# Optimization experiments

Measured on AMD Instinct MI355X. Metric: run time of the kernel, lower is better.

Reference implementation:

```python
import jax, jax.numpy as jnp
import numpy as np

B, L, H, E, K = 64, 200, 256, 8, 2
LN_EPS = 1e-5

def setup_inputs() -> dict:
    key = jax.random.key(0)
    ks = jax.random.split(key, 24)
    r = lambda k, *s: jax.random.normal(k, s, dtype=jnp.float32)
    w = lambda k, *s: 0.02 * jax.random.normal(k, s, dtype=jnp.float32)
    return {
        'text_emb': r(ks[0], B, L, H),
        'img_emb': r(ks[1], B, L, H),
        'item_emb': r(ks[2], B, L, H),
        'noise_t': r(ks[3], B, L, H),
        'noise_i': r(ks[4], B, L, H),
        'W_mu_t': w(ks[5], H, H), 'b_mu_t': jnp.zeros((H,), jnp.float32),
        'W_sg_t': w(ks[6], H, H), 'b_sg_t': jnp.zeros((H,), jnp.float32),
        'W_mu_i': w(ks[7], H, H), 'b_mu_i': jnp.zeros((H,), jnp.float32),
        'W_sg_i': w(ks[8], H, H), 'b_sg_i': jnp.zeros((H,), jnp.float32),
        'W_gate': w(ks[9], H, E), 'b_gate': jnp.zeros((E,), jnp.float32),
        'W_texp': w(ks[10], E, H, H), 'b_texp': jnp.zeros((E, H), jnp.float32),
        'W_iexp': w(ks[11], E, H, H), 'b_iexp': jnp.zeros((E, H), jnp.float32),
        'W_fuse': w(ks[12], 2 * H, H), 'b_fuse': jnp.zeros((H,), jnp.float32),
        'ln_g': jnp.ones((H,), jnp.float32), 'ln_b': jnp.zeros((H,), jnp.float32),
    }

def _topk_routing(z, W_gate, b_gate):
    # softmax over experts, keep top-k, renormalize (matches torch scatter_ version)
    weights = jax.nn.softmax(z @ W_gate + b_gate, axis=-1)   # [B,L,E]
    top_w, idx = jax.lax.top_k(weights, K)                   # [B,L,K]
    sparse = jnp.sum(jax.nn.one_hot(idx, E, dtype=weights.dtype) * top_w[..., None], axis=-2)
    return sparse / (jnp.sum(sparse, axis=-1, keepdims=True) + 1e-8)

def _layernorm(x, g, b):
    mu = jnp.mean(x, axis=-1, keepdims=True)
    var = jnp.mean(jnp.square(x - mu), axis=-1, keepdims=True)
    return (x - mu) * jax.lax.rsqrt(var + LN_EPS) * g + b

def reference(text_emb, img_emb, item_emb, noise_t, noise_i,
              W_mu_t, b_mu_t, W_sg_t, b_sg_t, W_mu_i, b_mu_i, W_sg_i, b_sg_i,
              W_gate, b_gate, W_texp, b_texp, W_iexp, b_iexp,
              W_fuse, b_fuse, ln_g, ln_b):
    # VAE-style reparameterization per modality
    t_mu = text_emb @ W_mu_t + b_mu_t
    t_sigma = jnp.exp(text_emb @ W_sg_t + b_sg_t)
    i_mu = img_emb @ W_mu_i + b_mu_i
    i_sigma = jnp.exp(img_emb @ W_sg_i + b_sg_i)
    t_z = t_mu + t_sigma * noise_t
    i_z = i_mu + i_sigma * noise_i
    # top-k gating
    t_gate = _topk_routing(t_z, W_gate, b_gate)   # [B,L,E]
    i_gate = _topk_routing(i_z, W_gate, b_gate)
    # dense all-expert stack + gated combine
    t_experts = jnp.einsum('blh,ehd->bled', t_z, W_texp) + b_texp  # [B,L,E,H]
    t_out = jnp.einsum('bled,ble->bld', t_experts, t_gate)
    i_experts = jnp.einsum('blh,ehd->bled', i_z, W_iexp) + b_iexp
    i_out = jnp.einsum('bled,ble->bld', i_experts, i_gate)
    # fusion: Linear(2H->H) -> LayerNorm -> ReLU, residual with item_emb
    cat = jnp.concatenate([t_out, i_out], axis=-1)
    fused = jax.nn.relu(_layernorm(cat @ W_fuse + b_fuse, ln_g, ln_b))
    fusion = item_emb + fused
    return fusion, t_mu, t_sigma, i_mu, i_sigma
```

## Files before the change

### kernel.cpp

```cpp
#include <hip/hip_runtime.h>
#include <hip/hip_bf16.h>
#include <math.h>

#define NTOK 12800
#define HD 256
#define SOUT (NTOK * HD)

typedef __attribute__((ext_vector_type(8))) short short8_t;
typedef __attribute__((ext_vector_type(4))) float f32x4;

__device__ __forceinline__ unsigned short f2b(float f) {
    union { float f; unsigned u; } v; v.f = f;
    unsigned r = (v.u + 0x7FFFu + ((v.u >> 16) & 1u)) >> 16;
    return (unsigned short)r;
}
__device__ __forceinline__ float b2f(unsigned short s) {
    union { unsigned u; float f; } v; v.u = ((unsigned)s) << 16;
    return v.f;
}

__global__ __launch_bounds__(256) void prepW_kernel(
    const float* __restrict__ W_texp, const float* __restrict__ W_iexp,
    const float* __restrict__ W_mu_t, const float* __restrict__ W_sg_t,
    const float* __restrict__ W_mu_i, const float* __restrict__ W_sg_i,
    const float* __restrict__ W_fuse,
    unsigned short* __restrict__ wt_t, unsigned short* __restrict__ wt_i,
    unsigned short* __restrict__ wt_f,
    unsigned short* __restrict__ wt_muth, unsigned short* __restrict__ wt_mutl,
    unsigned short* __restrict__ wt_sgth, unsigned short* __restrict__ wt_sgtl,
    unsigned short* __restrict__ wt_muih, unsigned short* __restrict__ wt_muil,
    unsigned short* __restrict__ wt_sgih, unsigned short* __restrict__ wt_sgil)
{
    const int z = blockIdx.y;
    const float* src;
    unsigned short* dsth;
    unsigned short* dstl = nullptr;
    int dstride = 256, koff = 0;
    if (z < 8)       { src = W_texp + (size_t)z * 65536;       dsth = wt_t + (size_t)z * 65536; }
    else if (z < 16) { src = W_iexp + (size_t)(z - 8) * 65536; dsth = wt_i + (size_t)(z - 8) * 65536; }
    else if (z == 16){ src = W_mu_t; dsth = wt_muth; dstl = wt_mutl; }
    else if (z == 17){ src = W_sg_t; dsth = wt_sgth; dstl = wt_sgtl; }
    else if (z == 18){ src = W_mu_i; dsth = wt_muih; dstl = wt_muil; }
    else if (z == 19){ src = W_sg_i; dsth = wt_sgih; dstl = wt_sgil; }
    else if (z == 20){ src = W_fuse;         dsth = wt_f; dstride = 512; koff = 0;   }
    else             { src = W_fuse + 65536; dsth = wt_f; dstride = 512; koff = 256; }

    const int tk = (blockIdx.x >> 2) * 64;
    const int td = (blockIdx.x & 3) * 64;
    __shared__ float T[64][68];
    const int t = threadIdx.x;
    {
        const int r = t >> 2, c0 = (t & 3) * 16;
        const float* s = &src[(size_t)(tk + r) * 256 + td + c0];
#pragma unroll
        for (int j = 0; j < 4; ++j)
            *reinterpret_cast<float4*>(&T[r][c0 + j * 4]) =
                *reinterpret_cast<const float4*>(&s[j * 4]);
    }
    __syncthreads();
    {
        const int d = t & 63, kc = (t >> 6) * 16;
        union { unsigned short s[16]; short8_t v[2]; } uh, ul;
#pragma unroll
        for (int j = 0; j < 16; ++j) {
            const float x = T[kc + j][d];
            uh.s[j] = f2b(x);
            ul.s[j] = f2b(x - b2f(uh.s[j]));
        }
        unsigned short* p = &dsth[(size_t)(td + d) * dstride + koff + tk + kc];
        *reinterpret_cast<short8_t*>(p) = uh.v[0];
        *reinterpret_cast<short8_t*>(p + 8) = uh.v[1];
        if (dstl) {
            unsigned short* q = &dstl[(size_t)(td + d) * 256 + tk + kc];
            *reinterpret_cast<short8_t*>(q) = ul.v[0];
            *reinterpret_cast<short8_t*>(q + 8) = ul.v[1];
        }
    }
}

__global__ __launch_bounds__(256) void reparam_mfma_kernel(
    const float* __restrict__ text, const float* __restrict__ img,
    const unsigned short* __restrict__ wt_muth, const unsigned short* __restrict__ wt_mutl,
    const unsigned short* __restrict__ wt_sgth, const unsigned short* __restrict__ wt_sgtl,
    const unsigned short* __restrict__ wt_muih, const unsigned short* __restrict__ wt_muil,
    const unsigned short* __restrict__ wt_sgih, const unsigned short* __restrict__ wt_sgil,
    const float* __restrict__ b_mu_t, const float* __restrict__ b_sg_t,
    const float* __restrict__ b_mu_i, const float* __restrict__ b_sg_i,
    const float* __restrict__ noise_t, const float* __restrict__ noise_i,
    float* __restrict__ o_tmu, float* __restrict__ o_tsig,
    float* __restrict__ o_imu, float* __restrict__ o_isig,
    unsigned short* __restrict__ tzb, unsigned short* __restrict__ izb)
{
    const int mod = blockIdx.z;
    const float* A            = mod ? img     : text;
    const unsigned short* Wmh = mod ? wt_muih : wt_muth;
    const unsigned short* Wml = mod ? wt_muil : wt_mutl;
    const unsigned short* Wsh = mod ? wt_sgih : wt_sgth;
    const unsigned short* Wsl = mod ? wt_sgil : wt_sgtl;
    const float* bmu          = mod ? b_mu_i  : b_mu_t;
    const float* bsg          = mod ? b_sg_i  : b_sg_t;
    const float* noise        = mod ? noise_i : noise_t;
    float* omu                = mod ? o_imu   : o_tmu;
    float* osg                = mod ? o_isig  : o_tsig;
    unsigned short* zb        = mod ? izb     : tzb;

    __shared__ __align__(16) unsigned short Ahs[4][128][8];
    __shared__ __align__(16) unsigned short Als[4][128][8];
    __shared__ __align__(16) unsigned short BMh[4][128][8];
    __shared__ __align__(16) unsigned short BMl[4][128][8];
    __shared__ __align__(16) unsigned short BSh[4][128][8];
    __shared__ __align__(16) unsigned short BSl[4][128][8];

    const int tid = threadIdx.x;
    const int lane = tid & 63;
    const int w = tid >> 6;
    const int wr = w >> 1, wc = w & 1;
    const int lg = lane >> 4;
    const int lr = lane & 15;
    const int m0 = blockIdx.x * 128;
    const int n0 = blockIdx.y * 128;

    f32x4 accM[4][4], accS[4][4];
#pragma unroll
    for (int mi = 0; mi < 4; ++mi)
#pragma unroll
        for (int ni = 0; ni < 4; ++ni) {
            accM[mi][ni] = (f32x4){0.f, 0.f, 0.f, 0.f};
            accS[mi][ni] = (f32x4){0.f, 0.f, 0.f, 0.f};
        }

    for (int ks = 0; ks < 8; ++ks) {
        __syncthreads();
        {
            const int r = tid >> 1, h = tid & 1;
            const float* s = &A[(size_t)(m0 + r) * HD + ks * 32 + h * 16];
#pragma unroll
            for (int j = 0; j < 2; ++j) {
                const float4 v0 = *reinterpret_cast<const float4*>(&s[j * 8]);
                const float4 v1 = *reinterpret_cast<const float4*>(&s[j * 8 + 4]);
                float x[8] = { v0.x, v0.y, v0.z, v0.w, v1.x, v1.y, v1.z, v1.w };
                union { unsigned short u[8]; short8_t v; } qh, ql;
#pragma unroll
                for (int c = 0; c < 8; ++c) {
                    qh.u[c] = f2b(x[c]);
                    ql.u[c] = f2b(x[c] - b2f(qh.u[c]));
                }
                *reinterpret_cast<short8_t*>(&Ahs[h * 2 + j][r][0]) = qh.v;
                *reinterpret_cast<short8_t*>(&Als[h * 2 + j][r][0]) = ql.v;
            }
        }
        {
            const int n = tid >> 1, h = tid & 1;
            const size_t wo = (size_t)(n0 + n) * HD + ks * 32 + h * 16;
#pragma unroll
            for (int j = 0; j < 2; ++j) {
                *reinterpret_cast<short8_t*>(&BMh[2 * h + j][n][0]) =
                    *reinterpret_cast<const short8_t*>(&Wmh[wo + j * 8]);
                *reinterpret_cast<short8_t*>(&BMl[2 * h + j][n][0]) =
                    *reinterpret_cast<const short8_t*>(&Wml[wo + j * 8]);
                *reinterpret_cast<short8_t*>(&BSh[2 * h + j][n][0]) =
                    *reinterpret_cast<const short8_t*>(&Wsh[wo + j * 8]);
                *reinterpret_cast<short8_t*>(&BSl[2 * h + j][n][0]) =
                    *reinterpret_cast<const short8_t*>(&Wsl[wo + j * 8]);
            }
        }
        __syncthreads();

        short8_t ahf[4], alf[4];
#pragma unroll
        for (int mi = 0; mi < 4; ++mi) {
            ahf[mi] = *reinterpret_cast<const short8_t*>(&Ahs[lg][wr * 64 + mi * 16 + lr][0]);
            alf[mi] = *reinterpret_cast<const short8_t*>(&Als[lg][wr * 64 + mi * 16 + lr][0]);
        }
#pragma unroll
        for (int ni = 0; ni < 4; ++ni) {
            const short8_t bmh = *reinterpret_cast<const short8_t*>(&BMh[lg][wc * 64 + ni * 16 + lr][0]);
            const short8_t bml = *reinterpret_cast<const short8_t*>(&BMl[lg][wc * 64 + ni * 16 + lr][0]);
            const short8_t bsh = *reinterpret_cast<const short8_t*>(&BSh[lg][wc * 64 + ni * 16 + lr][0]);
            const short8_t bsl = *reinterpret_cast<const short8_t*>(&BSl[lg][wc * 64 + ni * 16 + lr][0]);
#pragma unroll
            for (int mi = 0; mi < 4; ++mi) {
                accM[mi][ni] = __builtin_amdgcn_mfma_f32_16x16x32_bf16(ahf[mi], bmh, accM[mi][ni], 0, 0, 0);
                accM[mi][ni] = __builtin_amdgcn_mfma_f32_16x16x32_bf16(ahf[mi], bml, accM[mi][ni], 0, 0, 0);
                accM[mi][ni] = __builtin_amdgcn_mfma_f32_16x16x32_bf16(alf[mi], bmh, accM[mi][ni], 0, 0, 0);
                accS[mi][ni] = __builtin_amdgcn_mfma_f32_16x16x32_bf16(ahf[mi], bsh, accS[mi][ni], 0, 0, 0);
                accS[mi][ni] = __builtin_amdgcn_mfma_f32_16x16x32_bf16(ahf[mi], bsl, accS[mi][ni], 0, 0, 0);
                accS[mi][ni] = __builtin_amdgcn_mfma_f32_16x16x32_bf16(alf[mi], bsh, accS[mi][ni], 0, 0, 0);
            }
        }
    }

    float bm[4], bs[4];
    int cc[4];
#pragma unroll
    for (int ni = 0; ni < 4; ++ni) {
        cc[ni] = n0 + wc * 64 + ni * 16 + lr;
        bm[ni] = bmu[cc[ni]];
        bs[ni] = bsg[cc[ni]];
    }
#pragma unroll
    for (int mi = 0; mi < 4; ++mi) {
#pragma unroll
        for (int r = 0; r < 4; ++r) {
            const int row = m0 + wr * 64 + mi * 16 + lg * 4 + r;
#pragma unroll
            for (int ni = 0; ni < 4; ++ni) {
                const size_t off = (size_t)row * HD + cc[ni];
                const float mu = accM[mi][ni][r] + bm[ni];
                const float sg = expf(accS[mi][ni][r] + bs[ni]);
                omu[off] = mu;
                osg[off] = sg;
                zb[off] = f2b(fmaf(sg, noise[off], mu));
            }
        }
    }
}

__global__ __launch_bounds__(256) void gate_kernel(
    const float* __restrict__ mu, const float* __restrict__ sig,
    const float* __restrict__ noise, const float* __restrict__ Wg,
    const float* __restrict__ bg, float* __restrict__ gate)
{
    const int lane = threadIdx.x & 63;
    const int n = blockIdx.x * 4 + (threadIdx.x >> 6);
    const size_t off = (size_t)n * HD + lane * 4;
    const float4 m4 = *reinterpret_cast<const float4*>(&mu[off]);
    const float4 s4 = *reinterpret_cast<const float4*>(&sig[off]);
    const float4 n4 = *reinterpret_cast<const float4*>(&noise[off]);
    const float zz[4] = { fmaf(s4.x, n4.x, m4.x), fmaf(s4.y, n4.y, m4.y),
                          fmaf(s4.z, n4.z, m4.z), fmaf(s4.w, n4.w, m4.w) };
    float lg[8];
#pragma unroll
    for (int e = 0; e < 8; ++e) lg[e] = 0.f;
#pragma unroll
    for (int i = 0; i < 4; ++i) {
        const float* wr = &Wg[(size_t)(lane * 4 + i) * 8];
        const float4 w0 = *reinterpret_cast<const float4*>(wr);
        const float4 w1 = *reinterpret_cast<const float4*>(wr + 4);
        lg[0] = fmaf(zz[i], w0.x, lg[0]); lg[1] = fmaf(zz[i], w0.y, lg[1]);
        lg[2] = fmaf(zz[i], w0.z, lg[2]); lg[3] = fmaf(zz[i], w0.w, lg[3]);
        lg[4] = fmaf(zz[i], w1.x, lg[4]); lg[5] = fmaf(zz[i], w1.y, lg[5]);
        lg[6] = fmaf(zz[i], w1.z, lg[6]); lg[7] = fmaf(zz[i], w1.w, lg[7]);
    }
#pragma unroll
    for (int off2 = 32; off2; off2 >>= 1)
#pragma unroll
        for (int e = 0; e < 8; ++e) lg[e] += __shfl_down(lg[e], off2);

    if (lane == 0) {
        float m = -1e30f;
#pragma unroll
        for (int e = 0; e < 8; ++e) { lg[e] += bg[e]; m = fmaxf(m, lg[e]); }
        float p[8], s = 0.f;
// ... 13 lines not shown
#pragma unroll
        for (int e = 0; e < 8; ++e) g[e] = 0.f;
        g[e1] = p[e1] * denom; g[e2] = p[e2] * denom;
        float* gr = &gate[(size_t)n * 8];
        *reinterpret_cast<float4*>(gr)     = make_float4(g[0], g[1], g[2], g[3]);
        *reinterpret_cast<float4*>(gr + 4) = make_float4(g[4], g[5], g[6], g[7]);
    }
}

__global__ __launch_bounds__(256) void expert_mfma_kernel(
    const unsigned short* __restrict__ tzb, const unsigned short* __restrict__ izb,
    const unsigned short* __restrict__ wt_t, const unsigned short* __restrict__ wt_i,
    const float* __restrict__ bx_t, const float* __restrict__ bx_i,
    const float* __restrict__ g_t, const float* __restrict__ g_i,
    unsigned short* __restrict__ out_t, unsigned short* __restrict__ out_i)
{
    const int mod = blockIdx.z;
    const unsigned short* Zb = mod ? izb : tzb;
    const unsigned short* Wt = mod ? wt_i : wt_t;
    const float* bx   = mod ? bx_i : bx_t;
    const float* gate = mod ? g_i  : g_t;
    unsigned short* outp = mod ? out_i : out_t;

    __shared__ __align__(16) unsigned short Al[32][128][8];
    __shared__ __align__(16) unsigned short Bl[4][128][8];
    __shared__ float gld[128][8];

    const int tid = threadIdx.x;
    const int lane = tid & 63;
    const int w = tid >> 6;
    const int wr = w >> 1, wc = w & 1;
    const int lg = lane >> 4;
    const int lr = lane & 15;
    const int m0 = blockIdx.x * 128;
    const int n0 = blockIdx.y * 128;

    reinterpret_cast<float4*>(&gld[0][0])[tid] =
        reinterpret_cast<const float4*>(&gate[(size_t)m0 * 8])[tid];

    {
        const int r = tid >> 1, h = tid & 1;
        const unsigned short* src = &Zb[(size_t)(m0 + r) * HD + h * 128];
#pragma unroll
        for (int j = 0; j < 16; ++j)
            *reinterpret_cast<short8_t*>(&Al[h * 16 + j][r][0]) =
                *reinterpret_cast<const short8_t*>(&src[j * 8]);
    }
    __syncthreads();

    f32x4 accT[4][4];
#pragma unroll
    for (int mi = 0; mi < 4; ++mi)
#pragma unroll
        for (int ni = 0; ni < 4; ++ni)
            accT[mi][ni] = (f32x4){0.f, 0.f, 0.f, 0.f};

    for (int e = 0; e < 8; ++e) {
        f32x4 acc[4][4];
#pragma unroll
        for (int mi = 0; mi < 4; ++mi)
#pragma unroll
            for (int ni = 0; ni < 4; ++ni)
                acc[mi][ni] = (f32x4){0.f, 0.f, 0.f, 0.f};

        const unsigned short* We = &Wt[(size_t)e * HD * HD + (size_t)n0 * HD];

        for (int ks = 0; ks < 8; ++ks) {
            __syncthreads();
            {
                const int n = tid >> 1, h = tid & 1;
                const unsigned short* s = &We[(size_t)n * HD + ks * 32 + h * 16];
                *reinterpret_cast<short8_t*>(&Bl[2 * h][n][0]) =
                    *reinterpret_cast<const short8_t*>(&s[0]);
                *reinterpret_cast<short8_t*>(&Bl[2 * h + 1][n][0]) =
                    *reinterpret_cast<const short8_t*>(&s[8]);
            }
            __syncthreads();

            short8_t af[4], bf[4];
#pragma unroll
            for (int mi = 0; mi < 4; ++mi)
                af[mi] = *reinterpret_cast<const short8_t*>(
                    &Al[ks * 4 + lg][wr * 64 + mi * 16 + lr][0]);
#pragma unroll
            for (int ni = 0; ni < 4; ++ni)
                bf[ni] = *reinterpret_cast<const short8_t*>(
                    &Bl[lg][wc * 64 + ni * 16 + lr][0]);
#pragma unroll
            for (int mi = 0; mi < 4; ++mi)
#pragma unroll
                for (int ni = 0; ni < 4; ++ni)
                    acc[mi][ni] = __builtin_amdgcn_mfma_f32_16x16x32_bf16(
                        af[mi], bf[ni], acc[mi][ni], 0, 0, 0);
        }

#pragma unroll
        for (int mi = 0; mi < 4; ++mi) {
            const int rb = wr * 64 + mi * 16 + lg * 4;
            const float gv0 = gld[rb + 0][e];
            const float gv1 = gld[rb + 1][e];
            const float gv2 = gld[rb + 2][e];
            const float gv3 = gld[rb + 3][e];
#pragma unroll
            for (int ni = 0; ni < 4; ++ni) {
                const float bv = bx[(size_t)e * HD + n0 + wc * 64 + ni * 16 + lr];
                accT[mi][ni][0] += gv0 * (acc[mi][ni][0] + bv);
                accT[mi][ni][1] += gv1 * (acc[mi][ni][1] + bv);
                accT[mi][ni][2] += gv2 * (acc[mi][ni][2] + bv);
                accT[mi][ni][3] += gv3 * (acc[mi][ni][3] + bv);
            }
        }
    }

#pragma unroll
    for (int mi = 0; mi < 4; ++mi)
#pragma unroll
        for (int ni = 0; ni < 4; ++ni)
#pragma unroll
            for (int r = 0; r < 4; ++r)
                outp[(size_t)(m0 + wr * 64 + mi * 16 + lg * 4 + r) * HD
                     + n0 + wc * 64 + ni * 16 + lr] = f2b(accT[mi][ni][r]);
}

__global__ __launch_bounds__(256) void fusegemm_mfma_kernel(
    const unsigned short* __restrict__ t_outb, const unsigned short* __restrict__ i_outb,
    const unsigned short* __restrict__ wtf, const float* __restrict__ bfuse,
    float* __restrict__ fused)
{
    __shared__ __align__(16) unsigned short Al[8][128][8];
    __shared__ __align__(16) unsigned short Bl[8][128][8];

    const int tid = threadIdx.x;
    const int lane = tid & 63;
    const int w = tid >> 6;
    const int wr = w >> 1, wc = w & 1;
    const int lg = lane >> 4;
    const int lr = lane & 15;
    const int m0 = blockIdx.x * 128;
    const int n0 = blockIdx.y * 128;

    f32x4 acc[4][4];
#pragma unroll
    for (int mi = 0; mi < 4; ++mi)
#pragma unroll
        for (int ni = 0; ni < 4; ++ni)
            acc[mi][ni] = (f32x4){0.f, 0.f, 0.f, 0.f};

    for (int ks = 0; ks < 8; ++ks) {
        __syncthreads();
        {
            const int r = tid >> 1, h = tid & 1;
            const unsigned short* base = (ks < 4) ? t_outb : i_outb;
            const int kloc = (ks & 3) * 64 + h * 32;
            const unsigned short* s = &base[(size_t)(m0 + r) * HD + kloc];
#pragma unroll
            for (int j = 0; j < 4; ++j)
                *reinterpret_cast<short8_t*>(&Al[h * 4 + j][r][0]) =
                    *reinterpret_cast<const short8_t*>(&s[j * 8]);
        }
        {
            const int n = tid >> 1, h = tid & 1;
            const unsigned short* s = &wtf[(size_t)(n0 + n) * 512 + ks * 64 + h * 32];
#pragma unroll
            for (int j = 0; j < 4; ++j)
                *reinterpret_cast<short8_t*>(&Bl[h * 4 + j][n][0]) =
                    *reinterpret_cast<const short8_t*>(&s[j * 8]);
        }
        __syncthreads();

#pragma unroll
        for (int kc = 0; kc < 2; ++kc) {
            short8_t af[4], bf[4];
#pragma unroll
            for (int mi = 0; mi < 4; ++mi)
                af[mi] = *reinterpret_cast<const short8_t*>(
                    &Al[kc * 4 + lg][wr * 64 + mi * 16 + lr][0]);
#pragma unroll
            for (int ni = 0; ni < 4; ++ni)
                bf[ni] = *reinterpret_cast<const short8_t*>(
                    &Bl[kc * 4 + lg][wc * 64 + ni * 16 + lr][0]);
#pragma unroll
            for (int mi = 0; mi < 4; ++mi)
#pragma unroll
                for (int ni = 0; ni < 4; ++ni)
                    acc[mi][ni] = __builtin_amdgcn_mfma_f32_16x16x32_bf16(
                        af[mi], bf[ni], acc[mi][ni], 0, 0, 0);
        }
    }

    float bv[4];
    int cc[4];
#pragma unroll
    for (int ni = 0; ni < 4; ++ni) {
        cc[ni] = n0 + wc * 64 + ni * 16 + lr;
        bv[ni] = bfuse[cc[ni]];
    }
#pragma unroll
    for (int mi = 0; mi < 4; ++mi)
#pragma unroll
        for (int r = 0; r < 4; ++r) {
            const int row = m0 + wr * 64 + mi * 16 + lg * 4 + r;
#pragma unroll
            for (int ni = 0; ni < 4; ++ni)
                fused[(size_t)row * HD + cc[ni]] = acc[mi][ni][r] + bv[ni];
        }
}

__global__ __launch_bounds__(256) void ln_relu_res_kernel(
    const float* __restrict__ fused, const float* __restrict__ g,
    const float* __restrict__ b, const float* __restrict__ item,
    float* __restrict__ fusion)
{
    const int lane = threadIdx.x & 63;
    const int n = blockIdx.x * 4 + (threadIdx.x >> 6);
    const size_t off = (size_t)n * HD + lane * 4;
    const float4 x = *reinterpret_cast<const float4*>(&fused[off]);
    float s = x.x + x.y + x.z + x.w;
    float ss = x.x * x.x + x.y * x.y + x.z * x.z + x.w * x.w;
#pragma unroll
    for (int o = 32; o; o >>= 1) { s += __shfl_xor(s, o); ss += __shfl_xor(ss, o); }
    const float mean = s * (1.f / 256.f);
    const float var = ss * (1.f / 256.f) - mean * mean;
    const float rstd = rsqrtf(var + 1e-5f);
    const float4 gg = *reinterpret_cast<const float4*>(&g[lane * 4]);
// ... 22 lines not shown
    const float* b_sg_t  = (const float*)d_in[8];
    const float* W_mu_i  = (const float*)d_in[9];
    const float* b_mu_i  = (const float*)d_in[10];
    const float* W_sg_i  = (const float*)d_in[11];
    const float* b_sg_i  = (const float*)d_in[12];
    const float* W_gate  = (const float*)d_in[13];
    const float* b_gate  = (const float*)d_in[14];
    const float* W_texp  = (const float*)d_in[15];
    const float* b_texp  = (const float*)d_in[16];
    const float* W_iexp  = (const float*)d_in[17];
    const float* b_iexp  = (const float*)d_in[18];
    const float* W_fuse  = (const float*)d_in[19];
    const float* b_fuse  = (const float*)d_in[20];
    const float* ln_g    = (const float*)d_in[21];
    const float* ln_b    = (const float*)d_in[22];

    float* out    = (float*)d_out;
    float* fusion = out;
    float* o_tmu  = out + (size_t)SOUT;
    float* o_tsig = out + (size_t)2 * SOUT;
    float* o_imu  = out + (size_t)3 * SOUT;
    float* o_isig = out + (size_t)4 * SOUT;

    float* ws     = (float*)d_ws;
    float* fused  = ws;
    float* t_gate = ws + (size_t)SOUT;
    float* i_gate = t_gate + (size_t)NTOK * 8;
    unsigned short* tzb    = (unsigned short*)(i_gate + (size_t)NTOK * 8);
    unsigned short* izb    = tzb + (size_t)SOUT;
    unsigned short* t_outb = izb + (size_t)SOUT;
    unsigned short* i_outb = t_outb + (size_t)SOUT;
    unsigned short* wt_t   = i_outb + (size_t)SOUT;
    unsigned short* wt_i   = wt_t + (size_t)8 * 65536;
    unsigned short* wt_f   = wt_i + (size_t)8 * 65536;
    unsigned short* wt_muth = wt_f + (size_t)512 * 256;
    unsigned short* wt_mutl = wt_muth + 65536;
    unsigned short* wt_sgth = wt_mutl + 65536;
    unsigned short* wt_sgtl = wt_sgth + 65536;
    unsigned short* wt_muih = wt_sgtl + 65536;
    unsigned short* wt_muil = wt_muih + 65536;
    unsigned short* wt_sgih = wt_muil + 65536;
    unsigned short* wt_sgil = wt_sgih + 65536;

    prepW_kernel<<<dim3(16, 22), 256, 0, stream>>>(
        W_texp, W_iexp, W_mu_t, W_sg_t, W_mu_i, W_sg_i, W_fuse,
        wt_t, wt_i, wt_f,
        wt_muth, wt_mutl, wt_sgth, wt_sgtl,
        wt_muih, wt_muil, wt_sgih, wt_sgil);

    reparam_mfma_kernel<<<dim3(NTOK / 128, 2, 2), 256, 0, stream>>>(
        text, img,
        wt_muth, wt_mutl, wt_sgth, wt_sgtl,
        wt_muih, wt_muil, wt_sgih, wt_sgil,
        b_mu_t, b_sg_t, b_mu_i, b_sg_i, noise_t, noise_i,
        o_tmu, o_tsig, o_imu, o_isig, tzb, izb);

    gate_kernel<<<NTOK / 4, 256, 0, stream>>>(o_tmu, o_tsig, noise_t, W_gate, b_gate, t_gate);
    gate_kernel<<<NTOK / 4, 256, 0, stream>>>(o_imu, o_isig, noise_i, W_gate, b_gate, i_gate);

    expert_mfma_kernel<<<dim3(NTOK / 128, 2, 2), 256, 0, stream>>>(
        tzb, izb, wt_t, wt_i, b_texp, b_iexp, t_gate, i_gate, t_outb, i_outb);

    fusegemm_mfma_kernel<<<dim3(NTOK / 128, 2), 256, 0, stream>>>(
        t_outb, i_outb, wt_f, b_fuse, fused);

    ln_relu_res_kernel<<<NTOK / 4, 256, 0, stream>>>(fused, ln_g, ln_b, item, fusion);
}
```

Before: 165.6 us.

## Pre-split inputs to bf16 hi/lo, pack mu/sigma weights, double-buffer GEMMs with smaller tiles

Adds a conversion kernel that splits the text and image embeddings into bf16 hi/lo pairs once, so the reparam GEMM no longer converts them inside its K loop. The mu and sigma weights are packed into one 512-wide N dimension, so each reparam block computes either mu or sigma rather than both. The reparam, expert and fuse GEMMs move to 64-row tiles with register-staged double-buffered shared memory, one barrier per K step, and more blocks in flight. The z computation and bf16 store move into a single two-modality gate kernel, and workspace buffers are aliased to save memory. In exchange this adds an extra launch and a full read-write pass over the activations, and each weight tile is reloaded by more blocks.

```diff
diff --git a/kernel.cpp b/kernel.cpp
--- a/kernel.cpp
+++ b/kernel.cpp
@@ -26,22 +26,20 @@
     const float* __restrict__ W_fuse,
     unsigned short* __restrict__ wt_t, unsigned short* __restrict__ wt_i,
     unsigned short* __restrict__ wt_f,
-    unsigned short* __restrict__ wt_muth, unsigned short* __restrict__ wt_mutl,
-    unsigned short* __restrict__ wt_sgth, unsigned short* __restrict__ wt_sgtl,
-    unsigned short* __restrict__ wt_muih, unsigned short* __restrict__ wt_muil,
-    unsigned short* __restrict__ wt_sgih, unsigned short* __restrict__ wt_sgil)
+    unsigned short* __restrict__ wpk_th, unsigned short* __restrict__ wpk_tl,
+    unsigned short* __restrict__ wpk_ih, unsigned short* __restrict__ wpk_il)
 {
     const int z = blockIdx.y;
     const float* src;
     unsigned short* dsth;
     unsigned short* dstl = nullptr;
-    int dstride = 256, koff = 0;
+    int dstride = 256, koff = 0, rowoff = 0;
     if (z < 8)       { src = W_texp + (size_t)z * 65536;       dsth = wt_t + (size_t)z * 65536; }
     else if (z < 16) { src = W_iexp + (size_t)(z - 8) * 65536; dsth = wt_i + (size_t)(z - 8) * 65536; }
-    else if (z == 16){ src = W_mu_t; dsth = wt_muth; dstl = wt_mutl; }
-    else if (z == 17){ src = W_sg_t; dsth = wt_sgth; dstl = wt_sgtl; }
-    else if (z == 18){ src = W_mu_i; dsth = wt_muih; dstl = wt_muil; }
-    else if (z == 19){ src = W_sg_i; dsth = wt_sgih; dstl = wt_sgil; }
+    else if (z == 16){ src = W_mu_t; dsth = wpk_th; dstl = wpk_tl; }
+    else if (z == 17){ src = W_sg_t; dsth = wpk_th; dstl = wpk_tl; rowoff = 256; }
+    else if (z == 18){ src = W_mu_i; dsth = wpk_ih; dstl = wpk_il; }
+    else if (z == 19){ src = W_sg_i; dsth = wpk_ih; dstl = wpk_il; rowoff = 256; }
     else if (z == 20){ src = W_fuse;         dsth = wt_f; dstride = 512; koff = 0;   }
     else             { src = W_fuse + 65536; dsth = wt_f; dstride = 512; koff = 256; }
 
@@ -67,49 +65,64 @@
             uh.s[j] = f2b(x);
             ul.s[j] = f2b(x - b2f(uh.s[j]));
         }
-        unsigned short* p = &dsth[(size_t)(td + d) * dstride + koff + tk + kc];
+        unsigned short* p = &dsth[(size_t)(rowoff + td + d) * dstride + koff + tk + kc];
         *reinterpret_cast<short8_t*>(p) = uh.v[0];
         *reinterpret_cast<short8_t*>(p + 8) = uh.v[1];
         if (dstl) {
-            unsigned short* q = &dstl[(size_t)(td + d) * 256 + tk + kc];
+            unsigned short* q = &dstl[(size_t)(rowoff + td + d) * 256 + tk + kc];
             *reinterpret_cast<short8_t*>(q) = ul.v[0];
             *reinterpret_cast<short8_t*>(q + 8) = ul.v[1];
         }
     }
 }
 
+__global__ __launch_bounds__(256) void cvt_kernel(
+    const float* __restrict__ text, const float* __restrict__ img,
+    unsigned short* __restrict__ ah_t, unsigned short* __restrict__ al_t,
+    unsigned short* __restrict__ ah_i, unsigned short* __restrict__ al_i)
+{
+    const int mod = blockIdx.y;
+    const float* src = mod ? img : text;
+    unsigned short* dh = mod ? ah_i : ah_t;
+    unsigned short* dl = mod ? al_i : al_t;
+    const size_t base = ((size_t)blockIdx.x * 256 + threadIdx.x) * 8;
+    const float4 v0 = *reinterpret_cast<const float4*>(&src[base]);
+    const float4 v1 = *reinterpret_cast<const float4*>(&src[base + 4]);
+    const float x[8] = { v0.x, v0.y, v0.z, v0.w, v1.x, v1.y, v1.z, v1.w };
+    union { unsigned short u[8]; short8_t v; } qh, ql;
+#pragma unroll
+    for (int c = 0; c < 8; ++c) {
+        qh.u[c] = f2b(x[c]);
+        ql.u[c] = f2b(x[c] - b2f(qh.u[c]));
+    }
+    *reinterpret_cast<short8_t*>(&dh[base]) = qh.v;
+    *reinterpret_cast<short8_t*>(&dl[base]) = ql.v;
+}
+
 __global__ __launch_bounds__(256) void reparam_mfma_kernel(
-    const float* __restrict__ text, const float* __restrict__ img,
-    const unsigned short* __restrict__ wt_muth, const unsigned short* __restrict__ wt_mutl,
-    const unsigned short* __restrict__ wt_sgth, const unsigned short* __restrict__ wt_sgtl,
-    const unsigned short* __restrict__ wt_muih, const unsigned short* __restrict__ wt_muil,
-    const unsigned short* __restrict__ wt_sgih, const unsigned short* __restrict__ wt_sgil,
+    const unsigned short* __restrict__ ah_t, const unsigned short* __restrict__ al_t,
+    const unsigned short* __restrict__ ah_i, const unsigned short* __restrict__ al_i,
+    const unsigned short* __restrict__ wpk_th, const unsigned short* __restrict__ wpk_tl,
+    const unsigned short* __restrict__ wpk_ih, const unsigned short* __restrict__ wpk_il,
     const float* __restrict__ b_mu_t, const float* __restrict__ b_sg_t,
     const float* __restrict__ b_mu_i, const float* __restrict__ b_sg_i,
-    const float* __restrict__ noise_t, const float* __restrict__ noise_i,
     float* __restrict__ o_tmu, float* __restrict__ o_tsig,
-    float* __restrict__ o_imu, float* __restrict__ o_isig,
-    unsigned short* __restrict__ tzb, unsigned short* __restrict__ izb)
+    float* __restrict__ o_imu, float* __restrict__ o_isig)
 {
     const int mod = blockIdx.z;
-    const float* A            = mod ? img     : text;
-    const unsigned short* Wmh = mod ? wt_muih : wt_muth;
-    const unsigned short* Wml = mod ? wt_muil : wt_mutl;
-    const unsigned short* Wsh = mod ? wt_sgih : wt_sgth;
-    const unsigned short* Wsl = mod ? wt_sgil : wt_sgtl;
-    const float* bmu          = mod ? b_mu_i  : b_mu_t;
-    const float* bsg          = mod ? b_sg_i  : b_sg_t;
-    const float* noise        = mod ? noise_i : noise_t;
-    float* omu                = mod ? o_imu   : o_tmu;
-    float* osg                = mod ? o_isig  : o_tsig;
-    unsigned short* zb        = mod ? izb     : tzb;
-
-    __shared__ __align__(16) unsigned short Ahs[4][128][8];
-    __shared__ __align__(16) unsigned short Als[4][128][8];
-    __shared__ __align__(16) unsigned short BMh[4][128][8];
-    __shared__ __align__(16) unsigned short BMl[4][128][8];
-    __shared__ __align__(16) unsigned short BSh[4][128][8];
-    __shared__ __align__(16) unsigned short BSl[4][128][8];
+    const unsigned short* Ah = mod ? ah_i : ah_t;
+    const unsigned short* Al = mod ? al_i : al_t;
+    const unsigned short* Wh = mod ? wpk_ih : wpk_th;
+    const unsigned short* Wl = mod ? wpk_il : wpk_tl;
+    const float* bmu = mod ? b_mu_i : b_mu_t;
+    const float* bsg = mod ? b_sg_i : b_sg_t;
+    float* omu = mod ? o_imu : o_tmu;
+    float* osg = mod ? o_isig : o_tsig;
+
+    __shared__ __align__(16) unsigned short AhS[2][4][64][8];
+    __shared__ __align__(16) unsigned short AlS[2][4][64][8];
+    __shared__ __align__(16) unsigned short BhS[2][4][128][8];
+    __shared__ __align__(16) unsigned short BlS[2][4][128][8];
 
     const int tid = threadIdx.x;
     const int lane = tid & 63;
@@ -117,110 +130,120 @@
     const int wr = w >> 1, wc = w & 1;
     const int lg = lane >> 4;
     const int lr = lane & 15;
-    const int m0 = blockIdx.x * 128;
+    const int m0 = blockIdx.x * 64;
     const int n0 = blockIdx.y * 128;
 
-    f32x4 accM[4][4], accS[4][4];
-#pragma unroll
-    for (int mi = 0; mi < 4; ++mi)
+    const int ar = tid >> 2, akc = tid & 3;
+    const int bn = tid >> 1, bk0 = (tid & 1) * 2;
+
+    {
+        *reinterpret_cast<short8_t*>(&AhS[0][akc][ar][0]) =
+            *reinterpret_cast<const short8_t*>(&Ah[(size_t)(m0 + ar) * HD + akc * 8]);
+        *reinterpret_cast<short8_t*>(&AlS[0][akc][ar][0]) =
+            *reinterpret_cast<const short8_t*>(&Al[(size_t)(m0 + ar) * HD + akc * 8]);
+#pragma unroll
+        for (int j = 0; j < 2; ++j) {
+            const int kc = bk0 + j;
+            *reinterpret_cast<short8_t*>(&BhS[0][kc][bn][0]) =
+                *reinterpret_cast<const short8_t*>(&Wh[(size_t)(n0 + bn) * HD + kc * 8]);
+            *reinterpret_cast<short8_t*>(&BlS[0][kc][bn][0]) =
+                *reinterpret_cast<const short8_t*>(&Wl[(size_t)(n0 + bn) * HD + kc * 8]);
+        }
+    }
+    __syncthreads();
+
+    f32x4 acc[2][4];
+#pragma unroll
+    for (int mi = 0; mi < 2; ++mi)
+#pragma unroll
+        for (int ni = 0; ni < 4; ++ni)
+            acc[mi][ni] = (f32x4){0.f, 0.f, 0.f, 0.f};
+
+    for (int ks = 0; ks < 8; ++ks) {
+        const int cur = ks & 1;
+        short8_t rah, ral, rbh[2], rbl[2];
+        if (ks < 7) {
+            const int k1 = (ks + 1) * 32;
+            rah = *reinterpret_cast<const short8_t*>(&Ah[(size_t)(m0 + ar) * HD + k1 + akc * 8]);
+            ral = *reinterpret_cast<const short8_t*>(&Al[(size_t)(m0 + ar) * HD + k1 + akc * 8]);
+#pragma unroll
+            for (int j = 0; j < 2; ++j) {
+                const int kc = bk0 + j;
+                rbh[j] = *reinterpret_cast<const short8_t*>(&Wh[(size_t)(n0 + bn) * HD + k1 + kc * 8]);
+                rbl[j] = *reinterpret_cast<const short8_t*>(&Wl[(size_t)(n0 + bn) * HD + k1 + kc * 8]);
+            }
+        }
+        short8_t ahf[2], alf[2], bhf[4], blf[4];
+#pragma unroll
+        for (int mi = 0; mi < 2; ++mi) {
+            ahf[mi] = *reinterpret_cast<const short8_t*>(&AhS[cur][lg][wr * 32 + mi * 16 + lr][0]);
+            alf[mi] = *reinterpret_cast<const short8_t*>(&AlS[cur][lg][wr * 32 + mi * 16 + lr][0]);
+        }
 #pragma unroll
         for (int ni = 0; ni < 4; ++ni) {
-            accM[mi][ni] = (f32x4){0.f, 0.f, 0.f, 0.f};
-            accS[mi][ni] = (f32x4){0.f, 0.f, 0.f, 0.f};
-        }
-
-    for (int ks = 0; ks < 8; ++ks) {
+            bhf[ni] = *reinterpret_cast<const short8_t*>(&BhS[cur][lg][wc * 64 + ni * 16 + lr][0]);
+            blf[ni] = *reinterpret_cast<const short8_t*>(&BlS[cur][lg][wc * 64 + ni * 16 + lr][0]);
+        }
+#pragma unroll
+        for (int mi = 0; mi < 2; ++mi)
+#pragma unroll
+            for (int ni = 0; ni < 4; ++ni) {
+                acc[mi][ni] = __builtin_amdgcn_mfma_f32_16x16x32_bf16(ahf[mi], bhf[ni], acc[mi][ni], 0, 0, 0);
+                acc[mi][ni] = __builtin_amdgcn_mfma_f32_16x16x32_bf16(ahf[mi], blf[ni], acc[mi][ni], 0, 0, 0);
+                acc[mi][ni] = __builtin_amdgcn_mfma_f32_16x16x32_bf16(alf[mi], bhf[ni], acc[mi][ni], 0, 0, 0);
+            }
+        if (ks < 7) {
+            const int nxt = cur ^ 1;
+            *reinterpret_cast<short8_t*>(&AhS[nxt][akc][ar][0]) = rah;
+            *reinterpret_cast<short8_t*>(&AlS[nxt][akc][ar][0]) = ral;
+#pragma unroll
+            for (int j = 0; j < 2; ++j) {
+                const int kc = bk0 + j;
+                *reinterpret_cast<short8_t*>(&BhS[nxt][kc][bn][0]) = rbh[j];
+                *reinterpret_cast<short8_t*>(&BlS[nxt][kc][bn][0]) = rbl[j];
+            }
+        }
         __syncthreads();
-        {
-            const int r = tid >> 1, h = tid & 1;
-            const float* s = &A[(size_t)(m0 + r) * HD + ks * 32 + h * 16];
-#pragma unroll
-            for (int j = 0; j < 2; ++j) {
-                const float4 v0 = *reinterpret_cast<const float4*>(&s[j * 8]);
-                const float4 v1 = *reinterpret_cast<const float4*>(&s[j * 8 + 4]);
-                float x[8] = { v0.x, v0.y, v0.z, v0.w, v1.x, v1.y, v1.z, v1.w };
-                union { unsigned short u[8]; short8_t v; } qh, ql;
-#pragma unroll
-                for (int c = 0; c < 8; ++c) {
-                    qh.u[c] = f2b(x[c]);
-                    ql.u[c] = f2b(x[c] - b2f(qh.u[c]));
-                }
-                *reinterpret_cast<short8_t*>(&Ahs[h * 2 + j][r][0]) = qh.v;
-                *reinterpret_cast<short8_t*>(&Als[h * 2 + j][r][0]) = ql.v;
-            }
-        }
-        {
-            const int n = tid >> 1, h = tid & 1;
-            const size_t wo = (size_t)(n0 + n) * HD + ks * 32 + h * 16;
-#pragma unroll
-            for (int j = 0; j < 2; ++j) {
-                *reinterpret_cast<short8_t*>(&BMh[2 * h + j][n][0]) =
-                    *reinterpret_cast<const short8_t*>(&Wmh[wo + j * 8]);
-                *reinterpret_cast<short8_t*>(&BMl[2 * h + j][n][0]) =
-                    *reinterpret_cast<const short8_t*>(&Wml[wo + j * 8]);
-                *reinterpret_cast<short8_t*>(&BSh[2 * h + j][n][0]) =
-                    *reinterpret_cast<const short8_t*>(&Wsh[wo + j * 8]);
-                *reinterpret_cast<short8_t*>(&BSl[2 * h + j][n][0]) =
-                    *reinterpret_cast<const short8_t*>(&Wsl[wo + j * 8]);
-            }
-        }
-        __syncthreads();
-
-        short8_t ahf[4], alf[4];
-#pragma unroll
-        for (int mi = 0; mi < 4; ++mi) {
-            ahf[mi] = *reinterpret_cast<const short8_t*>(&Ahs[lg][wr * 64 + mi * 16 + lr][0]);
-            alf[mi] = *reinterpret_cast<const short8_t*>(&Als[lg][wr * 64 + mi * 16 + lr][0]);
-        }
-#pragma unroll
-        for (int ni = 0; ni < 4; ++ni) {
-            const short8_t bmh = *reinterpret_cast<const short8_t*>(&BMh[lg][wc * 64 + ni * 16 + lr][0]);
-            const short8_t bml = *reinterpret_cast<const short8_t*>(&BMl[lg][wc * 64 + ni * 16 + lr][0]);
-            const short8_t bsh = *reinterpret_cast<const short8_t*>(&BSh[lg][wc * 64 + ni * 16 + lr][0]);
-            const short8_t bsl = *reinterpret_cast<const short8_t*>(&BSl[lg][wc * 64 + ni * 16 + lr][0]);
-#pragma unroll
-            for (int mi = 0; mi < 4; ++mi) {
-                accM[mi][ni] = __builtin_amdgcn_mfma_f32_16x16x32_bf16(ahf[mi], bmh, accM[mi][ni], 0, 0, 0);
-                accM[mi][ni] = __builtin_amdgcn_mfma_f32_16x16x32_bf16(ahf[mi], bml, accM[mi][ni], 0, 0, 0);
-                accM[mi][ni] = __builtin_amdgcn_mfma_f32_16x16x32_bf16(alf[mi], bmh, accM[mi][ni], 0, 0, 0);
-                accS[mi][ni] = __builtin_amdgcn_mfma_f32_16x16x32_bf16(ahf[mi], bsh, accS[mi][ni], 0, 0, 0);
-                accS[mi][ni] = __builtin_amdgcn_mfma_f32_16x16x32_bf16(ahf[mi], bsl, accS[mi][ni], 0, 0, 0);
-                accS[mi][ni] = __builtin_amdgcn_mfma_f32_16x16x32_bf16(alf[mi], bsh, accS[mi][ni], 0, 0, 0);
-            }
-        }
-    }
-
-    float bm[4], bs[4];
+    }
+
+    const bool is_sg = (n0 >= 256);
+    float bv[4];
     int cc[4];
 #pragma unroll
     for (int ni = 0; ni < 4; ++ni) {
-        cc[ni] = n0 + wc * 64 + ni * 16 + lr;
-        bm[ni] = bmu[cc[ni]];
-        bs[ni] = bsg[cc[ni]];
-    }
-#pragma unroll
-    for (int mi = 0; mi < 4; ++mi) {
+        const int dpk = n0 + wc * 64 + ni * 16 + lr;
+        cc[ni] = is_sg ? dpk - 256 : dpk;
+        bv[ni] = is_sg ? bsg[cc[ni]] : bmu[cc[ni]];
+    }
+    float* outp = is_sg ? osg : omu;
+#pragma unroll
+    for (int mi = 0; mi < 2; ++mi)
 #pragma unroll
         for (int r = 0; r < 4; ++r) {
-            const int row = m0 + wr * 64 + mi * 16 + lg * 4 + r;
+            const int row = m0 + wr * 32 + mi * 16 + lg * 4 + r;
 #pragma unroll
             for (int ni = 0; ni < 4; ++ni) {
-                const size_t off = (size_t)row * HD + cc[ni];
-                const float mu = accM[mi][ni][r] + bm[ni];
-                const float sg = expf(accS[mi][ni][r] + bs[ni]);
-                omu[off] = mu;
-                osg[off] = sg;
-                zb[off] = f2b(fmaf(sg, noise[off], mu));
-            }
-        }
-    }
+                const float v = acc[mi][ni][r] + bv[ni];
+                outp[(size_t)row * HD + cc[ni]] = is_sg ? expf(v) : v;
+            }
+        }
 }
 
 __global__ __launch_bounds__(256) void gate_kernel(
-    const float* __restrict__ mu, const float* __restrict__ sig,
-    const float* __restrict__ noise, const float* __restrict__ Wg,
-    const float* __restrict__ bg, float* __restrict__ gate)
-{
+    const float* __restrict__ o_tmu, const float* __restrict__ o_tsig,
+    const float* __restrict__ o_imu, const float* __restrict__ o_isig,
+    const float* __restrict__ noise_t, const float* __restrict__ noise_i,
+    const float* __restrict__ Wg, const float* __restrict__ bg,
+    float* __restrict__ t_gate, float* __restrict__ i_gate,
+    unsigned short* __restrict__ tzb, unsigned short* __restrict__ izb)
+{
+    const int mod = blockIdx.y;
+    const float* mu    = mod ? o_imu  : o_tmu;
+    const float* sig   = mod ? o_isig : o_tsig;
+    const float* noise = mod ? noise_i : noise_t;
+    float* gate        = mod ? i_gate : t_gate;
+    unsigned short* zb = mod ? izb : tzb;
+
     const int lane = threadIdx.x & 63;
     const int n = blockIdx.x * 4 + (threadIdx.x >> 6);
     const size_t off = (size_t)n * HD + lane * 4;
@@ -229,6 +252,10 @@
     const float4 n4 = *reinterpret_cast<const float4*>(&noise[off]);
     const float zz[4] = { fmaf(s4.x, n4.x, m4.x), fmaf(s4.y, n4.y, m4.y),
                           fmaf(s4.z, n4.z, m4.z), fmaf(s4.w, n4.w, m4.w) };
+    ushort4 zb4;
+    zb4.x = f2b(zz[0]); zb4.y = f2b(zz[1]); zb4.z = f2b(zz[2]); zb4.w = f2b(zz[3]);
+    *reinterpret_cast<ushort4*>(&zb[off]) = zb4;
+
     float lg[8];
 #pragma unroll
     for (int e = 0; e < 8; ++e) lg[e] = 0.f;
@@ -288,9 +315,9 @@
     const float* gate = mod ? g_i  : g_t;
     unsigned short* outp = mod ? out_i : out_t;
 
-    __shared__ __align__(16) unsigned short Al[32][128][8];
-    __shared__ __align__(16) unsigned short Bl[4][128][8];
-    __shared__ float gld[128][8];
+    __shared__ __align__(16) unsigned short AlS[32][64][8];
+    __shared__ __align__(16) unsigned short BlS[2][4][128][8];
+    __shared__ float gld[64][8];
 
     const int tid = threadIdx.x;
     const int lane = tid & 63;
@@ -298,93 +325,106 @@
     const int wr = w >> 1, wc = w & 1;
     const int lg = lane >> 4;
     const int lr = lane & 15;
-    const int m0 = blockIdx.x * 128;
+    const int m0 = blockIdx.x * 64;
     const int n0 = blockIdx.y * 128;
 
-    reinterpret_cast<float4*>(&gld[0][0])[tid] =
-        reinterpret_cast<const float4*>(&gate[(size_t)m0 * 8])[tid];
+    const int bn = tid >> 1, bk0 = (tid & 1) * 2;
 
     {
-        const int r = tid >> 1, h = tid & 1;
-        const unsigned short* src = &Zb[(size_t)(m0 + r) * HD + h * 128];
-#pragma unroll
-        for (int j = 0; j < 16; ++j)
-            *reinterpret_cast<short8_t*>(&Al[h * 16 + j][r][0]) =
+        const int r = tid >> 2, kcg = tid & 3;
+        const unsigned short* src = &Zb[(size_t)(m0 + r) * HD + kcg * 64];
+#pragma unroll
+        for (int j = 0; j < 8; ++j)
+            *reinterpret_cast<short8_t*>(&AlS[kcg * 8 + j][r][0]) =
                 *reinterpret_cast<const short8_t*>(&src[j * 8]);
     }
+    if (tid < 128)
+        reinterpret_cast<float4*>(&gld[0][0])[tid] =
+            reinterpret_cast<const float4*>(&gate[(size_t)m0 * 8])[tid];
+    {
+        const unsigned short* We = Wt + (size_t)n0 * HD;
+#pragma unroll
+        for (int j = 0; j < 2; ++j) {
+            const int kc = bk0 + j;
+            *reinterpret_cast<short8_t*>(&BlS[0][kc][bn][0]) =
+                *reinterpret_cast<const short8_t*>(&We[(size_t)bn * HD + kc * 8]);
+        }
+    }
     __syncthreads();
 
-    f32x4 accT[4][4];
-#pragma unroll
-    for (int mi = 0; mi < 4; ++mi)
+    f32x4 acc[2][4], accT[2][4];
+#pragma unroll
+    for (int mi = 0; mi < 2; ++mi)
+#pragma unroll
+        for (int ni = 0; ni < 4; ++ni) {
+            acc[mi][ni]  = (f32x4){0.f, 0.f, 0.f, 0.f};
+            accT[mi][ni] = (f32x4){0.f, 0.f, 0.f, 0.f};
+        }
+
+    for (int kk = 0; kk < 64; ++kk) {
+        const int cur = kk & 1;
+        const int e = kk >> 3, ks = kk & 7;
+        short8_t rb[2];
+        if (kk < 63) {
+            const int e2 = (kk + 1) >> 3, ks2 = (kk + 1) & 7;
+            const unsigned short* We2 = Wt + (size_t)e2 * HD * HD + (size_t)n0 * HD;
+#pragma unroll
+            for (int j = 0; j < 2; ++j) {
+                const int kc = bk0 + j;
+                rb[j] = *reinterpret_cast<const short8_t*>(
+                    &We2[(size_t)bn * HD + ks2 * 32 + kc * 8]);
+            }
+        }
+        short8_t af[2], bf[4];
+#pragma unroll
+        for (int mi = 0; mi < 2; ++mi)
+            af[mi] = *reinterpret_cast<const short8_t*>(
+                &AlS[ks * 4 + lg][wr * 32 + mi * 16 + lr][0]);
 #pragma unroll
         for (int ni = 0; ni < 4; ++ni)
-            accT[mi][ni] = (f32x4){0.f, 0.f, 0.f, 0.f};
-
-    for (int e = 0; e < 8; ++e) {
-        f32x4 acc[4][4];
-#pragma unroll
-        for (int mi = 0; mi < 4; ++mi)
+            bf[ni] = *reinterpret_cast<const short8_t*>(
+                &BlS[cur][lg][wc * 64 + ni * 16 + lr][0]);
+#pragma unroll
+        for (int mi = 0; mi < 2; ++mi)
 #pragma unroll
             for (int ni = 0; ni < 4; ++ni)
-                acc[mi][ni] = (f32x4){0.f, 0.f, 0.f, 0.f};
-
-        const unsigned short* We = &Wt[(size_t)e * HD * HD + (size_t)n0 * HD];
-
-        for (int ks = 0; ks < 8; ++ks) {
-            __syncthreads();
-            {
-                const int n = tid >> 1, h = tid & 1;
-                const unsigned short* s = &We[(size_t)n * HD + ks * 32 + h * 16];
-                *reinterpret_cast<short8_t*>(&Bl[2 * h][n][0]) =
-                    *reinterpret_cast<const short8_t*>(&s[0]);
-                *reinterpret_cast<short8_t*>(&Bl[2 * h + 1][n][0]) =
-                    *reinterpret_cast<const short8_t*>(&s[8]);
-            }
-            __syncthreads();
-
-            short8_t af[4], bf[4];
-#pragma unroll
-            for (int mi = 0; mi < 4; ++mi)
-                af[mi] = *reinterpret_cast<const short8_t*>(
-                    &Al[ks * 4 + lg][wr * 64 + mi * 16 + lr][0]);
-#pragma unroll
-            for (int ni = 0; ni < 4; ++ni)
-                bf[ni] = *reinterpret_cast<const short8_t*>(
-                    &Bl[lg][wc * 64 + ni * 16 + lr][0]);
-#pragma unroll
-            for (int mi = 0; mi < 4; ++mi)
-#pragma unroll
-                for (int ni = 0; ni < 4; ++ni)
-                    acc[mi][ni] = __builtin_amdgcn_mfma_f32_16x16x32_bf16(
-                        af[mi], bf[ni], acc[mi][ni], 0, 0, 0);
-        }
-
-#pragma unroll
-        for (int mi = 0; mi < 4; ++mi) {
-            const int rb = wr * 64 + mi * 16 + lg * 4;
-            const float gv0 = gld[rb + 0][e];
-            const float gv1 = gld[rb + 1][e];
-            const float gv2 = gld[rb + 2][e];
-            const float gv3 = gld[rb + 3][e];
-#pragma unroll
-            for (int ni = 0; ni < 4; ++ni) {
-                const float bv = bx[(size_t)e * HD + n0 + wc * 64 + ni * 16 + lr];
-                accT[mi][ni][0] += gv0 * (acc[mi][ni][0] + bv);
-                accT[mi][ni][1] += gv1 * (acc[mi][ni][1] + bv);
-                accT[mi][ni][2] += gv2 * (acc[mi][ni][2] + bv);
-                accT[mi][ni][3] += gv3 * (acc[mi][ni][3] + bv);
-            }
-        }
-    }
-
-#pragma unroll
-    for (int mi = 0; mi < 4; ++mi)
+                acc[mi][ni] = __builtin_amdgcn_mfma_f32_16x16x32_bf16(
+                    af[mi], bf[ni], acc[mi][ni], 0, 0, 0);
+        if (kk < 63) {
+            const int nxt = cur ^ 1;
+#pragma unroll
+            for (int j = 0; j < 2; ++j)
+                *reinterpret_cast<short8_t*>(&BlS[nxt][bk0 + j][bn][0]) = rb[j];
+        }
+        if (ks == 7) {
+#pragma unroll
+            for (int mi = 0; mi < 2; ++mi) {
+                const int rb2 = wr * 32 + mi * 16 + lg * 4;
+                const float gv0 = gld[rb2 + 0][e];
+                const float gv1 = gld[rb2 + 1][e];
+                const float gv2 = gld[rb2 + 2][e];
+                const float gv3 = gld[rb2 + 3][e];
+#pragma unroll
+                for (int ni = 0; ni < 4; ++ni) {
+                    const float bv = bx[(size_t)e * HD + n0 + wc * 64 + ni * 16 + lr];
+                    accT[mi][ni][0] += gv0 * (acc[mi][ni][0] + bv);
+                    accT[mi][ni][1] += gv1 * (acc[mi][ni][1] + bv);
+                    accT[mi][ni][2] += gv2 * (acc[mi][ni][2] + bv);
+                    accT[mi][ni][3] += gv3 * (acc[mi][ni][3] + bv);
+                    acc[mi][ni] = (f32x4){0.f, 0.f, 0.f, 0.f};
+                }
+            }
+        }
+        __syncthreads();
+    }
+
+#pragma unroll
+    for (int mi = 0; mi < 2; ++mi)
 #pragma unroll
         for (int ni = 0; ni < 4; ++ni)
 #pragma unroll
             for (int r = 0; r < 4; ++r)
-                outp[(size_t)(m0 + wr * 64 + mi * 16 + lg * 4 + r) * HD
+                outp[(size_t)(m0 + wr * 32 + mi * 16 + lg * 4 + r) * HD
                      + n0 + wc * 64 + ni * 16 + lr] = f2b(accT[mi][ni][r]);
 }
 
@@ -393,8 +433,8 @@
     const unsigned short* __restrict__ wtf, const float* __restrict__ bfuse,
     float* __restrict__ fused)
 {
-    __shared__ __align__(16) unsigned short Al[8][128][8];
-    __shared__ __align__(16) unsigned short Bl[8][128][8];
+    __shared__ __align__(16) unsigned short AS[2][8][64][8];
+    __shared__ __align__(16) unsigned short BS[2][8][128][8];
 
     const int tid = threadIdx.x;
     const int lane = tid & 63;
@@ -402,56 +442,84 @@
     const int wr = w >> 1, wc = w & 1;
     const int lg = lane >> 4;
     const int lr = lane & 15;
-    const int m0 = blockIdx.x * 128;
+    const int m0 = blockIdx.x * 64;
     const int n0 = blockIdx.y * 128;
 
-    f32x4 acc[4][4];
-#pragma unroll
-    for (int mi = 0; mi < 4; ++mi)
+    const int ar = tid >> 2, akc0 = (tid & 3) * 2;
+    const int bn = tid >> 1, bkc0 = (tid & 1) * 4;
+
+    {
+        const unsigned short* base = t_outb;
+#pragma unroll
+        for (int j = 0; j < 2; ++j) {
+            const int kc = akc0 + j;
+            *reinterpret_cast<short8_t*>(&AS[0][kc][ar][0]) =
+                *reinterpret_cast<const short8_t*>(&base[(size_t)(m0 + ar) * HD + kc * 8]);
+        }
+#pragma unroll
+        for (int j = 0; j < 4; ++j) {
+            const int kc = bkc0 + j;
+            *reinterpret_cast<short8_t*>(&BS[0][kc][bn][0]) =
+                *reinterpret_cast<const short8_t*>(&wtf[(size_t)(n0 + bn) * 512 + kc * 8]);
+        }
+    }
+    __syncthreads();
+
+    f32x4 acc[2][4];
+#pragma unroll
+    for (int mi = 0; mi < 2; ++mi)
 #pragma unroll
         for (int ni = 0; ni < 4; ++ni)
             acc[mi][ni] = (f32x4){0.f, 0.f, 0.f, 0.f};
 
     for (int ks = 0; ks < 8; ++ks) {
-        __syncthreads();
-        {
-            const int r = tid >> 1, h = tid & 1;
-            const unsigned short* base = (ks < 4) ? t_outb : i_outb;
-            const int kloc = (ks & 3) * 64 + h * 32;
-            const unsigned short* s = &base[(size_t)(m0 + r) * HD + kloc];
-#pragma unroll
-            for (int j = 0; j < 4; ++j)
-                *reinterpret_cast<short8_t*>(&Al[h * 4 + j][r][0]) =
-                    *reinterpret_cast<const short8_t*>(&s[j * 8]);
-        }
-        {
-            const int n = tid >> 1, h = tid & 1;
-            const unsigned short* s = &wtf[(size_t)(n0 + n) * 512 + ks * 64 + h * 32];
-#pragma unroll
-            for (int j = 0; j < 4; ++j)
-                *reinterpret_cast<short8_t*>(&Bl[h * 4 + j][n][0]) =
-                    *reinterpret_cast<const short8_t*>(&s[j * 8]);
-        }
-        __syncthreads();
-
-#pragma unroll
-        for (int kc = 0; kc < 2; ++kc) {
-            short8_t af[4], bf[4];
-#pragma unroll
-            for (int mi = 0; mi < 4; ++mi)
+        const int cur = ks & 1;
+        short8_t ra[2], rbv[4];
+        if (ks < 7) {
+            const int ks2 = ks + 1;
+            const unsigned short* base = (ks2 < 4) ? t_outb : i_outb;
+            const int kloc = (ks2 & 3) * 64;
+#pragma unroll
+            for (int j = 0; j < 2; ++j) {
+                const int kc = akc0 + j;
+                ra[j] = *reinterpret_cast<const short8_t*>(
+                    &base[(size_t)(m0 + ar) * HD + kloc + kc * 8]);
+            }
+#pragma unroll
+            for (int j = 0; j < 4; ++j) {
+                const int kc = bkc0 + j;
+                rbv[j] = *reinterpret_cast<const short8_t*>(
+                    &wtf[(size_t)(n0 + bn) * 512 + ks2 * 64 + kc * 8]);
+            }
+        }
+#pragma unroll
+        for (int s = 0; s < 2; ++s) {
+            short8_t af[2], bf[4];
+#pragma unroll
+            for (int mi = 0; mi < 2; ++mi)
                 af[mi] = *reinterpret_cast<const short8_t*>(
-                    &Al[kc * 4 + lg][wr * 64 + mi * 16 + lr][0]);
+                    &AS[cur][s * 4 + lg][wr * 32 + mi * 16 + lr][0]);
 #pragma unroll
             for (int ni = 0; ni < 4; ++ni)
                 bf[ni] = *reinterpret_cast<const short8_t*>(
-                    &Bl[kc * 4 + lg][wc * 64 + ni * 16 + lr][0]);
-#pragma unroll
-            for (int mi = 0; mi < 4; ++mi)
+                    &BS[cur][s * 4 + lg][wc * 64 + ni * 16 + lr][0]);
+#pragma unroll
+            for (int mi = 0; mi < 2; ++mi)
 #pragma unroll
                 for (int ni = 0; ni < 4; ++ni)
                     acc[mi][ni] = __builtin_amdgcn_mfma_f32_16x16x32_bf16(
                         af[mi], bf[ni], acc[mi][ni], 0, 0, 0);
         }
+        if (ks < 7) {
+            const int nxt = cur ^ 1;
+#pragma unroll
+            for (int j = 0; j < 2; ++j)
+                *reinterpret_cast<short8_t*>(&AS[nxt][akc0 + j][ar][0]) = ra[j];
+#pragma unroll
+            for (int j = 0; j < 4; ++j)
+                *reinterpret_cast<short8_t*>(&BS[nxt][bkc0 + j][bn][0]) = rbv[j];
+        }
+        __syncthreads();
     }
 
     float bv[4];
@@ -462,10 +530,10 @@
         bv[ni] = bfuse[cc[ni]];
     }
 #pragma unroll
-    for (int mi = 0; mi < 4; ++mi)
+    for (int mi = 0; mi < 2; ++mi)
 #pragma unroll
         for (int r = 0; r < 4; ++r) {
-            const int row = m0 + wr * 64 + mi * 16 + lg * 4 + r;
+            const int row = m0 + wr * 32 + mi * 16 + lg * 4 + r;
 #pragma unroll
             for (int ni = 0; ni < 4; ++ni)
                 fused[(size_t)row * HD + cc[ni]] = acc[mi][ni][r] + bv[ni];
@@ -534,46 +602,49 @@
     float* o_imu  = out + (size_t)3 * SOUT;
     float* o_isig = out + (size_t)4 * SOUT;
 
-    float* ws     = (float*)d_ws;
-    float* fused  = ws;
-    float* t_gate = ws + (size_t)SOUT;
+    unsigned short* bufA = (unsigned short*)d_ws;
+    unsigned short* bufB = bufA + (size_t)SOUT;
+    unsigned short* bufC = bufB + (size_t)SOUT;
+    unsigned short* tzb  = bufC + (size_t)2 * SOUT;
+    unsigned short* izb  = tzb + (size_t)SOUT;
+    float* t_gate = (float*)(izb + (size_t)SOUT);
     float* i_gate = t_gate + (size_t)NTOK * 8;
-    unsigned short* tzb    = (unsigned short*)(i_gate + (size_t)NTOK * 8);
-    unsigned short* izb    = tzb + (size_t)SOUT;
-    unsigned short* t_outb = izb + (size_t)SOUT;
-    unsigned short* i_outb = t_outb + (size_t)SOUT;
-    unsigned short* wt_t   = i_outb + (size_t)SOUT;
+    unsigned short* wt_t   = (unsigned short*)(i_gate + (size_t)NTOK * 8);
     unsigned short* wt_i   = wt_t + (size_t)8 * 65536;
     unsigned short* wt_f   = wt_i + (size_t)8 * 65536;
-    unsigned short* wt_muth = wt_f + (size_t)512 * 256;
-    unsigned short* wt_mutl = wt_muth + 65536;
-    unsigned short* wt_sgth = wt_mutl + 65536;
-    unsigned short* wt_sgtl = wt_sgth + 65536;
-    unsigned short* wt_muih = wt_sgtl + 65536;
-    unsigned short* wt_muil = wt_muih + 65536;
-    unsigned short* wt_sgih = wt_muil + 65536;
-    unsigned short* wt_sgil = wt_sgih + 65536;
+    unsigned short* wpk_th = wt_f + (size_t)131072;
+    unsigned short* wpk_tl = wpk_th + (size_t)131072;
+    unsigned short* wpk_ih = wpk_tl + (size_t)131072;
+    unsigned short* wpk_il = wpk_ih + (size_t)131072;
+
+    unsigned short* ah_t = bufA;
+    unsigned short* al_t = bufB;
+    unsigned short* ah_i = bufC;
+    unsigned short* al_i = bufC + (size_t)SOUT;
+    unsigned short* t_outb = bufA;
+    unsigned short* i_outb = bufB;
+    float* fused = (float*)bufC;
 
     prepW_kernel<<<dim3(16, 22), 256, 0, stream>>>(
         W_texp, W_iexp, W_mu_t, W_sg_t, W_mu_i, W_sg_i, W_fuse,
-        wt_t, wt_i, wt_f,
-        wt_muth, wt_mutl, wt_sgth, wt_sgtl,
-        wt_muih, wt_muil, wt_sgih, wt_sgil);
-
-    reparam_mfma_kernel<<<dim3(NTOK / 128, 2, 2), 256, 0, stream>>>(
-        text, img,
-        wt_muth, wt_mutl, wt_sgth, wt_sgtl,
-        wt_muih, wt_muil, wt_sgih, wt_sgil,
-        b_mu_t, b_sg_t, b_mu_i, b_sg_i, noise_t, noise_i,
-        o_tmu, o_tsig, o_imu, o_isig, tzb, izb);
-
-    gate_kernel<<<NTOK / 4, 256, 0, stream>>>(o_tmu, o_tsig, noise_t, W_gate, b_gate, t_gate);
-    gate_kernel<<<NTOK / 4, 256, 0, stream>>>(o_imu, o_isig, noise_i, W_gate, b_gate, i_gate);
-
-    expert_mfma_kernel<<<dim3(NTOK / 128, 2, 2), 256, 0, stream>>>(
+        wt_t, wt_i, wt_f, wpk_th, wpk_tl, wpk_ih, wpk_il);
+
+    cvt_kernel<<<dim3(SOUT / 2048, 2), 256, 0, stream>>>(
+        text, img, ah_t, al_t, ah_i, al_i);
+
+    reparam_mfma_kernel<<<dim3(NTOK / 64, 4, 2), 256, 0, stream>>>(
+        ah_t, al_t, ah_i, al_i, wpk_th, wpk_tl, wpk_ih, wpk_il,
+        b_mu_t, b_sg_t, b_mu_i, b_sg_i,
+        o_tmu, o_tsig, o_imu, o_isig);
+
+    gate_kernel<<<dim3(NTOK / 4, 2), 256, 0, stream>>>(
+        o_tmu, o_tsig, o_imu, o_isig, noise_t, noise_i,
+        W_gate, b_gate, t_gate, i_gate, tzb, izb);
+
+    expert_mfma_kernel<<<dim3(NTOK / 64, 2, 2), 256, 0, stream>>>(
         tzb, izb, wt_t, wt_i, b_texp, b_iexp, t_gate, i_gate, t_outb, i_outb);
 
-    fusegemm_mfma_kernel<<<dim3(NTOK / 128, 2), 256, 0, stream>>>(
+    fusegemm_mfma_kernel<<<dim3(NTOK / 64, 2), 256, 0, stream>>>(
         t_outb, i_outb, wt_f, b_fuse, fused);
 
     ln_relu_res_kernel<<<NTOK / 4, 256, 0, stream>>>(fused, ln_g, ln_b, item, fusion);
```

New measurement: 161.2 us. -2.7%, faster.
